# Kernel tuning notes

Measured on AMD Instinct MI355X. Metric: run time of the kernel, lower is better.

## Reference

```python
import jax, jax.numpy as jnp
from jax import lax
import numpy as np

T, B, P, A = 1000, 8192, 1024, 4
ER_DECAY = 1.0 - 1e-3  # per-trial exploration-rate decay


def setup_inputs() -> dict:
    key = jax.random.key(0)
    k1, k2, k3, k4 = jax.random.split(key, 4)
    params = jax.random.normal(k1, (13, P), dtype=jnp.float32) * 0.5
    choices = jax.random.randint(k2, (T, B), 0, A, dtype=jnp.int32)
    rewards = (jax.random.uniform(k3, (T, B)) < 0.5).astype(jnp.float32)
    pids = jax.random.randint(k4, (B,), 0, P, dtype=jnp.int32)
    return {"params": params, "rewards": rewards, "choices": choices, "pids": pids}


def _transform_params(params, pids):
    p = jnp.clip(params, -5.0, 5.0)
    sp, sg = jax.nn.softplus, jax.nn.sigmoid
    beta_r = jnp.clip(sp(p[0]), 0.01, 20.0)[pids]
    lapse = jnp.clip(sg(p[1]), 0.01, 0.99)[pids]
    prior = jnp.clip(sp(p[2]), 0.01, 0.99)[pids]
    alpha_er = jnp.clip(sg(p[3]), 0.01, 0.99)[pids]
    decay = jnp.clip(sg(p[4]), 0.01, 0.99)[pids]
    ab1 = p[5][pids]
    ab2 = p[6][pids]
    perv = sp(p[7])[pids]
    sw = p[8][pids]
    gam = sp(p[10])[pids]
    temp = jnp.clip(sp(p[11]) + 1e-6, 1e-6, 100.0)[pids]
    beta_p = sp(p[12])[pids]
    return beta_r, lapse, prior, alpha_er, decay, ab1, ab2, perv, sw, gam, temp, beta_p


def _forward(params, rewards, choices, pids):
    (beta_r, lapse, prior, alpha_er, decay, ab1, ab2,
     perv, sw, gam, temp, beta_p) = _transform_params(params, pids)
    nB = rewards.shape[1]

    q0 = prior[:, None] * jnp.ones((nB, A), dtype=rewards.dtype)
    carry0 = (q0,
              -jnp.ones((nB,), jnp.int32),          # old_choice
              jnp.zeros((nB,), rewards.dtype),       # trials since last switch
              alpha_er,                              # exploration rate
              jnp.zeros((nB, A), rewards.dtype))     # cumulative choice counts

    def step(carry, xs):
        q, old_choice, tsls, er, cum = carry
        choice, reward = xs                       # (B,), (B,)
        oh = jax.nn.one_hot(choice, A, dtype=q.dtype)        # (B, A)
        target = reward - gam * (1.0 - reward)                # loss-averse target
        q = q * (1.0 - oh) + oh * target[:, None]             # q[choice] = target
        same = choice == old_choice
        tsls = jnp.where(same, tsls + 1.0, 0.0)
        er = er * ER_DECAY
        cum = cum + oh
        # exploration smoothing toward mean, then decay
        q = (1.0 - er)[:, None] * q + er[:, None] * q.mean(-1, keepdims=True)
        q = q * decay[:, None]
        sm_in = beta_r[:, None] * q / temp[:, None] + beta_p[:, None] * jnp.log1p(cum)
        probs = (1.0 - lapse)[:, None] * jax.nn.softmax(sm_in, axis=-1) + lapse[:, None] / A
        cl = jnp.log(probs)
        samef = same.astype(q.dtype)[:, None]
        cl = (cl
              + samef * perv[:, None] * oh
              + (1.0 - samef) * sw[:, None] * oh
              + ab1[:, None] * jax.nn.one_hot(old_choice, A, dtype=q.dtype)  # old_choice=-1 -> zeros
              + ab2[:, None] * jax.nn.one_hot((choice + 2) % A, A, dtype=q.dtype)
              + oh * jnp.log(tsls + 1.0)[:, None])
        return (q, choice, tsls, er, cum), cl

    _, logits = lax.scan(step, carry0, (choices, rewards))
    return logits  # (T, B, A)


def reference(params, rewards, choices, pids):
    return _forward(params, rewards, choices, pids)
```

## Files before the change

kernel.cpp:

```cpp
#include <hip/hip_runtime.h>
#include <stdint.h>

#define T_TRIALS 1000
#define B_SIZE   8192
#define P_SIZE   1024
#define CHUNK    32
#define KCH      32
#define NM       31
#define BPB      16
#define BP       17
#define ER_DECAY 0.999f
#define ER_L2D   (-1.4434228e-3f)
#define LOG2E_F 1.4426950408889634f
#define LN2_F   0.69314718055994531f

typedef float f32x4_t __attribute__((ext_vector_type(4)));

__device__ __forceinline__ float sp_(float x){ return __logf(1.0f + __expf(x)); }
__device__ __forceinline__ float sg_(float x){ return 1.0f / (1.0f + __expf(-x)); }
__device__ __forceinline__ float clampf(float x, float lo, float hi){ return fminf(fmaxf(x, lo), hi); }

__global__ __launch_bounds__(512)
void castro_fused4(const float* __restrict__ params,
                   const float* __restrict__ rewards,
                   const int*   __restrict__ choices,
                   const int*   __restrict__ pids,
                   float4*      __restrict__ out4)
{
    __shared__ float4   smap0[NM][BP];
    __shared__ float4   smap1[NM][BP];
    __shared__ float4   smap2[NM][BP];
    __shared__ float4   smap3[NM][BP];
    __shared__ float4   smap4[NM][BP];
    __shared__ uint32_t smeta[NM][BP];
    __shared__ float    pshare[BPB][10];

    const int tid = threadIdx.x;
    const int k   = tid >> 4;
    const int bi  = tid & 15;
    const int b   = blockIdx.x * BPB + bi;
    const int t0  = k * CHUNK;
    const int pid = pids[b];

    const float p3  = clampf(params[ 3 * P_SIZE + pid], -5.0f, 5.0f);
    const float p4  = clampf(params[ 4 * P_SIZE + pid], -5.0f, 5.0f);
    const float p10 = clampf(params[10 * P_SIZE + pid], -5.0f, 5.0f);
    const float alpha_er = clampf(sg_(p3), 0.01f, 0.99f);
    const float decay    = clampf(sg_(p4), 0.01f, 0.99f);
    const float gam      = sp_(p10);
    const float gp1      = 1.0f + gam;

    if (tid < BPB) {
        const float q0_ = clampf(params[ 0 * P_SIZE + pid], -5.0f, 5.0f);
        const float q1_ = clampf(params[ 1 * P_SIZE + pid], -5.0f, 5.0f);
        const float q2_ = clampf(params[ 2 * P_SIZE + pid], -5.0f, 5.0f);
        const float q5_ = clampf(params[ 5 * P_SIZE + pid], -5.0f, 5.0f);
        const float q6_ = clampf(params[ 6 * P_SIZE + pid], -5.0f, 5.0f);
        const float q7_ = clampf(params[ 7 * P_SIZE + pid], -5.0f, 5.0f);
        const float q8_ = clampf(params[ 8 * P_SIZE + pid], -5.0f, 5.0f);
        const float q11 = clampf(params[11 * P_SIZE + pid], -5.0f, 5.0f);
        const float q12 = clampf(params[12 * P_SIZE + pid], -5.0f, 5.0f);
        const float beta_r = clampf(sp_(q0_), 0.01f, 20.0f);
        const float lapse  = clampf(sg_(q1_), 0.01f, 0.99f);
        const float prior  = clampf(sp_(q2_), 0.01f, 0.99f);
        const float temp   = clampf(sp_(q11) + 1e-6f, 1e-6f, 100.0f);
        pshare[tid][0] = (beta_r / temp) * LOG2E_F;
        pshare[tid][1] = 1.0f - lapse;
        pshare[tid][2] = 0.25f * lapse;
        pshare[tid][3] = prior;
        pshare[tid][4] = sp_(q7_);
        pshare[tid][5] = q8_;
        pshare[tid][6] = q5_;
        pshare[tid][7] = q6_;
        pshare[tid][8] = sp_(q12);
        pshare[tid][9] = 0.0f;
    }

    const int*   cp = choices + (size_t)t0 * B_SIZE + b;
    const float* rp = rewards + (size_t)t0 * B_SIZE + b;

    uint32_t wr[4] = {0u, 0u, 0u, 0u};

    if (k < NM) {
        float er = alpha_er * exp2f((float)t0 * ER_L2D);

        float m00=1.f,m01=0.f,m02=0.f,m03=0.f;
        float m10=0.f,m11=1.f,m12=0.f,m13=0.f;
        float m20=0.f,m21=0.f,m22=1.f,m23=0.f;
        float m30=0.f,m31=0.f,m32=0.f,m33=1.f;
        float b0=0.f,b1=0.f,b2=0.f,b3=0.f;
        int   c1=0,c2=0,c3=0;
        int   run=0, last=-1;

        int cbuf[8]; float rbuf[8];
        #pragma unroll
        for (int i = 0; i < 8; ++i) {
            cbuf[i] = cp[(size_t)i * B_SIZE];
            rbuf[i] = rp[(size_t)i * B_SIZE];
        }

        #pragma unroll
        for (int g = 0; g < 4; ++g) {
            int cc[8]; float rr[8];
            #pragma unroll
            for (int i = 0; i < 8; ++i) { cc[i]=cbuf[i]; rr[i]=rbuf[i]; }
            if (g < 3) {
                #pragma unroll
                for (int i = 0; i < 8; ++i) {
                    cbuf[i] = cp[(size_t)((g+1)*8 + i) * B_SIZE];
                    rbuf[i] = rp[(size_t)((g+1)*8 + i) * B_SIZE];
                }
            }
            uint32_t gw = 0;
            #pragma unroll
            for (int i = 0; i < 8; ++i) {
                const int   c = cc[i];
                const float r = rr[i];
                gw |= ((uint32_t)c | (r > 0.5f ? 4u : 0u)) << (4*i);

                er *= ER_DECAY;
                const float target = fmaf(r, gp1, -gam);
                const bool e0=(c==0), e1=(c==1), e2=(c==2), e3=(c==3);

                m00=e0?0.f:m00; m01=e0?0.f:m01; m02=e0?0.f:m02; m03=e0?0.f:m03; b0=e0?target:b0;
                m10=e1?0.f:m10; m11=e1?0.f:m11; m12=e1?0.f:m12; m13=e1?0.f:m13; b1=e1?target:b1;
                m20=e2?0.f:m20; m21=e2?0.f:m21; m22=e2?0.f:m22; m23=e2?0.f:m23; b2=e2?target:b2;
                m30=e3?0.f:m30; m31=e3?0.f:m31; m32=e3?0.f:m32; m33=e3?0.f:m33; b3=e3?target:b3;

                const float s0=(m00+m10)+(m20+m30);
                const float s1=(m01+m11)+(m21+m31);
                const float s2=(m02+m12)+(m22+m32);
                const float s3=(m03+m13)+(m23+m33);
                const float sb=(b0+b1)+(b2+b3);
                const float a  = decay * (1.0f - er);
                const float e4 = decay * er * 0.25f;

                m00=fmaf(e4,s0,a*m00); m01=fmaf(e4,s1,a*m01); m02=fmaf(e4,s2,a*m02); m03=fmaf(e4,s3,a*m03);
                m10=fmaf(e4,s0,a*m10); m11=fmaf(e4,s1,a*m11); m12=fmaf(e4,s2,a*m12); m13=fmaf(e4,s3,a*m13);
                m20=fmaf(e4,s0,a*m20); m21=fmaf(e4,s1,a*m21); m22=fmaf(e4,s2,a*m22); m23=fmaf(e4,s3,a*m23);
                m30=fmaf(e4,s0,a*m30); m31=fmaf(e4,s1,a*m31); m32=fmaf(e4,s2,a*m32); m33=fmaf(e4,s3,a*m33);
                b0=fmaf(e4,sb,a*b0); b1=fmaf(e4,sb,a*b1); b2=fmaf(e4,sb,a*b2); b3=fmaf(e4,sb,a*b3);

                c1 += e1; c2 += e2; c3 += e3;
                run = (c == last) ? run + 1 : 1;
                last = c;
            }
            wr[g] = gw;
        }

        smap0[k][bi] = make_float4(m00,m01,m02,m03);
        smap1[k][bi] = make_float4(m10,m11,m12,m13);
        smap2[k][bi] = make_float4(m20,m21,m22,m23);
        smap3[k][bi] = make_float4(m30,m31,m32,m33);
        smap4[k][bi] = make_float4(b0,b1,b2,b3);
        smeta[k][bi] = (uint32_t)c1 | ((uint32_t)c2<<6) | ((uint32_t)c3<<12)
                     | ((uint32_t)last<<18) | ((uint32_t)run<<20);
    } else {
        uint32_t gw = 0;
        #pragma unroll
        for (int i = 0; i < 8; ++i) {
            const int   c = cp[(size_t)i * B_SIZE];
            const float r = rp[(size_t)i * B_SIZE];
            gw |= ((uint32_t)c | (r > 0.5f ? 4u : 0u)) << (4*i);
        }
        wr[0] = gw;
    }

    __syncthreads();

    if (tid < BPB) {
        const float prior = pshare[tid][3];
        float q0=prior, q1=prior, q2=prior, q3=prior;
        int n0=0,n1=0,n2=0,n3=0;
        int g_run=0, g_last=-1;

        for (int k2 = 0; k2 < KCH; ++k2) {
            if (k2 > 0) {
                const int tsls = g_run - 1;
                smap0[k2-1][tid] = make_float4(q0,q1,q2,q3);
                smap1[k2-1][tid] = make_float4(0.0f,
                                               __int_as_float(n0 | (n1<<16)),
                                               __int_as_float(n2 | (n3<<16)),
                                               __int_as_float((tsls & 0xFFFF) | (g_last<<16)));
            }
            if (k2 < NM) {
                const float4 r0 = smap0[k2][tid];
                const float4 r1 = smap1[k2][tid];
                const float4 r2 = smap2[k2][tid];
                const float4 r3 = smap3[k2][tid];
                const float4 r4 = smap4[k2][tid];
                const uint32_t m = smeta[k2][tid];
                const float nq0 = fmaf(r0.w,q3, fmaf(r0.z,q2, fmaf(r0.y,q1, fmaf(r0.x,q0, r4.x))));
                const float nq1 = fmaf(r1.w,q3, fmaf(r1.z,q2, fmaf(r1.y,q1, fmaf(r1.x,q0, r4.y))));
                const float nq2 = fmaf(r2.w,q3, fmaf(r2.z,q2, fmaf(r2.y,q1, fmaf(r2.x,q0, r4.z))));
                const float nq3 = fmaf(r3.w,q3, fmaf(r3.z,q2, fmaf(r3.y,q1, fmaf(r3.x,q0, r4.w))));
                q0=nq0; q1=nq1; q2=nq2; q3=nq3;

                const int cc1 = (int)( m        & 63u);
                const int cc2 = (int)((m >> 6 ) & 63u);
                const int cc3 = (int)((m >> 12) & 63u);
                n0 += CHUNK - cc1 - cc2 - cc3;
                n1 += cc1; n2 += cc2; n3 += cc3;
                const int last = (int)((m >> 18) & 3u);
                const int rn   = (int)((m >> 20) & 63u);
                g_run  = (rn == CHUNK && last == g_last) ? g_run + CHUNK : rn;
                g_last = last;
            }
        }
    }
    __syncthreads();

    {
        const float bt2    = pshare[bi][0];
        const float ol     = pshare[bi][1];
        const float la4    = pshare[bi][2];
        const float prior  = pshare[bi][3];
        const float perv   = pshare[bi][4];
        const float sw     = pshare[bi][5];
        const float ab1    = pshare[bi][6];
        const float ab2    = pshare[bi][7];
        const float beta_p = pshare[bi][8];

        float q0,q1,q2,q3, ft;
        float f0,f1,f2,f3;
        int   old_c;
        if (k == 0) {
            q0=q1=q2=q3=prior; f0=f1=f2=f3=0.f; ft=0.f; old_c=-1;
        } else {
            const float4 sA = smap0[k-1][bi];
            const float4 sB = smap1[k-1][bi];
            q0=sA.x; q1=sA.y; q2=sA.z; q3=sA.w;
            const int u1 = __float_as_int(sB.y);
            const int u2 = __float_as_int(sB.z);
            const int u3 = __float_as_int(sB.w);
            f0 = (float)(u1 & 0xFFFF); f1 = (float)(u1 >> 16);
            f2 = (float)(u2 & 0xFFFF); f3 = (float)(u2 >> 16);
            ft = (float)(u3 & 0xFFFF);
            old_c = u3 >> 16;
        }
        float er = alpha_er * exp2f((float)t0 * ER_L2D);

        float bpl0 = beta_p * __log2f(1.0f + f0);
        float bpl1 = beta_p * __log2f(1.0f + f1);
        float bpl2 = beta_p * __log2f(1.0f + f2);
        float bpl3 = beta_p * __log2f(1.0f + f3);

        float4* op = out4 + (size_t)t0 * B_SIZE + b;
        const int ngroups = (k == NM) ? 1 : 4;

        #pragma unroll
        for (int g = 0; g < 4; ++g) {
            if (g < ngroups) {
                uint32_t word = wr[g];
                #pragma unroll
                for (int i = 0; i < 8; ++i) {
                    const int   code = (int)(word & 0xFu); word >>= 4;
                    const int   c    = code & 3;
                    const float r    = (float)((code >> 2) & 1);

                    const float target = fmaf(r, gp1, -gam);
                    const bool e0=(c==0), e1=(c==1), e2=(c==2), e3=(c==3);
                    q0 = e0 ? target : q0;
                    q1 = e1 ? target : q1;
                    q2 = e2 ? target : q2;
                    q3 = e3 ? target : q3;

                    const bool same = (c == old_c);
                    ft = same ? ft + 1.0f : 0.0f;
                    er *= ER_DECAY;

                    const float fsel = e0 ? f0 : (e1 ? f1 : (e2 ? f2 : f3));
                    const float bplc = beta_p * __log2f(fsel + 2.0f);
                    f0 += e0 ? 1.0f : 0.0f;
                    f1 += e1 ? 1.0f : 0.0f;
                    f2 += e2 ? 1.0f : 0.0f;
                    f3 += e3 ? 1.0f : 0.0f;
                    bpl0 = e0 ? bplc : bpl0;
                    bpl1 = e1 ? bplc : bpl1;
                    bpl2 = e2 ? bplc : bpl2;
                    bpl3 = e3 ? bplc : bpl3;

                    const float qm = 0.25f * ((q0+q1)+(q2+q3));
                    q0 = decay * fmaf(er, qm - q0, q0);
                    q1 = decay * fmaf(er, qm - q1, q1);
                    q2 = decay * fmaf(er, qm - q2, q2);
                    q3 = decay * fmaf(er, qm - q3, q3);

                    const float s0 = fmaf(bt2, q0, bpl0);
                    const float s1 = fmaf(bt2, q1, bpl1);
                    const float s2 = fmaf(bt2, q2, bpl2);
                    const float s3 = fmaf(bt2, q3, bpl3);

                    const float m  = fmaxf(fmaxf(s0, s1), fmaxf(s2, s3));
                    const float x0 = exp2f(s0 - m);
                    const float x1 = exp2f(s1 - m);
                    const float x2 = exp2f(s2 - m);
                    const float x3 = exp2f(s3 - m);
                    const float inv = __builtin_amdgcn_rcpf((x0+x1)+(x2+x3));
                    const float sc  = ol * inv;

                    const float L0 = __log2f(fmaf(sc, x0, la4));
                    const float L1 = __log2f(fmaf(sc, x1, la4));
                    const float L2 = __log2f(fmaf(sc, x2, la4));
                    const float L3 = __log2f(fmaf(sc, x3, la4));

                    const float bonus = fmaf(LN2_F, __log2f(ft + 1.0f), same ? perv : sw);

                    float a0 = (e0 ? bonus : 0.0f) + ((old_c == 0) ? ab1 : 0.0f);
                    float a1 = (e1 ? bonus : 0.0f) + ((old_c == 1) ? ab1 : 0.0f);
                    float a2 = (e2 ? bonus : 0.0f) + ((old_c == 2) ? ab1 : 0.0f);
                    float a3 = (e3 ? bonus : 0.0f) + ((old_c == 3) ? ab1 : 0.0f);
                    const int c2 = (c + 2) & 3;
                    a0 += (c2 == 0) ? ab2 : 0.0f;
                    a1 += (c2 == 1) ? ab2 : 0.0f;
                    a2 += (c2 == 2) ? ab2 : 0.0f;
                    a3 += (c2 == 3) ? ab2 : 0.0f;

                    f32x4_t v = { fmaf(LN2_F, L0, a0), fmaf(LN2_F, L1, a1),
                                  fmaf(LN2_F, L2, a2), fmaf(LN2_F, L3, a3) };
                    __builtin_nontemporal_store(v,
                        reinterpret_cast<f32x4_t*>(op + (size_t)(g*8 + i) * B_SIZE));
                    old_c = c;
                }
            }
        }
    }
}

extern "C" void kernel_launch(void* const* d_in, const int* in_sizes, int n_in,
                              void* d_out, int out_size, void* d_ws, size_t ws_size,
                              hipStream_t stream)
{
    const float* params  = (const float*)d_in[0];
    const float* rewards = (const float*)d_in[1];
    const int*   choices = (const int*)  d_in[2];
    const int*   pids    = (const int*)  d_in[3];

    hipLaunchKernelGGL(castro_fused4, dim3(B_SIZE/BPB), dim3(512), 0, stream,
                       params, rewards, choices, pids, (float4*)d_out);
}
```

Before: 62.25 us.

## Add 1024-thread kernel with 16-trial chunks and dynamic LDS scan

Adds a new kernel that splits the 1000-trial scan into 16-trial chunks across 1024 threads per block (63 chunk-threads per batch element). Each chunk builds an affine transition map that a single thread composes serially, followed by a parallel replay that writes the logits. The host raises the dynamic shared memory limit to about 80 KB and falls back to the old 512-thread kernel if that call fails. Halving the chunk length shortens the per-thread serial replay, but it doubles the length of the serial composition and raises LDS use, which may lower occupancy.

```diff
diff --git a/kernel.cpp b/kernel.cpp
--- a/kernel.cpp
+++ b/kernel.cpp
@@ -4,21 +4,390 @@
 #define T_TRIALS 1000
 #define B_SIZE   8192
 #define P_SIZE   1024
+#define ER_DECAY 0.999f
+#define ER_L2D   (-1.4434228e-3f)
+#define LOG2E_F 1.4426950408889634f
+#define LN2_F   0.69314718055994531f
+
+typedef float f32x4_t __attribute__((ext_vector_type(4)));
+
+__device__ __forceinline__ float sp_(float x){ return __logf(1.0f + __expf(x)); }
+__device__ __forceinline__ float sg_(float x){ return 1.0f / (1.0f + __expf(-x)); }
+__device__ __forceinline__ float clampf(float x, float lo, float hi){ return fminf(fmaxf(x, lo), hi); }
+
+#define F5_CHUNK  16
+#define F5_NMST   60
+#define F5_LDS_BYTES 81536
+
+__global__ __launch_bounds__(1024, 8)
+void castro_fused5(const float* __restrict__ params,
+                   const float* __restrict__ rewards,
+                   const int*   __restrict__ choices,
+                   const int*   __restrict__ pids,
+                   float4*      __restrict__ out4)
+{
+    extern __shared__ char lds_raw[];
+    float4*   smap0  = (float4*)lds_raw;
+    float4*   smap1  = smap0 + 960;
+    float4*   smap2  = smap1 + 960;
+    float4*   smap3  = smap2 + 960;
+    float4*   smap4  = smap3 + 960;
+    uint32_t* smeta  = (uint32_t*)(smap4 + 960);
+    float*    pshare = (float*)(smeta + 960);
+    uint32_t* tailw  = (uint32_t*)(pshare + 160);
+
+    const int tid = threadIdx.x;
+    const int k   = tid >> 4;
+    const int bi  = tid & 15;
+    const int b   = blockIdx.x * 16 + bi;
+    const int t0  = k * F5_CHUNK;
+    const int pid = pids[b];
+
+    const float p3  = clampf(params[ 3 * P_SIZE + pid], -5.0f, 5.0f);
+    const float p4  = clampf(params[ 4 * P_SIZE + pid], -5.0f, 5.0f);
+    const float p10 = clampf(params[10 * P_SIZE + pid], -5.0f, 5.0f);
+    const float alpha_er = clampf(sg_(p3), 0.01f, 0.99f);
+    const float decay    = clampf(sg_(p4), 0.01f, 0.99f);
+    const float gam      = sp_(p10);
+    const float gp1      = 1.0f + gam;
+
+    if (tid < 16) {
+        const float q0_ = clampf(params[ 0 * P_SIZE + pid], -5.0f, 5.0f);
+        const float q1_ = clampf(params[ 1 * P_SIZE + pid], -5.0f, 5.0f);
+        const float q2_ = clampf(params[ 2 * P_SIZE + pid], -5.0f, 5.0f);
+        const float q5_ = clampf(params[ 5 * P_SIZE + pid], -5.0f, 5.0f);
+        const float q6_ = clampf(params[ 6 * P_SIZE + pid], -5.0f, 5.0f);
+        const float q7_ = clampf(params[ 7 * P_SIZE + pid], -5.0f, 5.0f);
+        const float q8_ = clampf(params[ 8 * P_SIZE + pid], -5.0f, 5.0f);
+        const float q11 = clampf(params[11 * P_SIZE + pid], -5.0f, 5.0f);
+        const float q12 = clampf(params[12 * P_SIZE + pid], -5.0f, 5.0f);
+        const float beta_r = clampf(sp_(q0_), 0.01f, 20.0f);
+        const float lapse  = clampf(sg_(q1_), 0.01f, 0.99f);
+        const float prior  = clampf(sp_(q2_), 0.01f, 0.99f);
+        const float temp   = clampf(sp_(q11) + 1e-6f, 1e-6f, 100.0f);
+        float* ps = pshare + tid * 10;
+        ps[0] = (beta_r / temp) * LOG2E_F;
+        ps[1] = 1.0f - lapse;
+        ps[2] = 0.25f * lapse;
+        ps[3] = prior;
+        ps[4] = sp_(q7_);
+        ps[5] = q8_;
+        ps[6] = q5_;
+        ps[7] = q6_;
+        ps[8] = sp_(q12);
+        ps[9] = 0.0f;
+    }
+
+    const int*   cp = choices + (size_t)t0 * B_SIZE + b;
+    const float* rp = rewards + (size_t)t0 * B_SIZE + b;
+
+    uint32_t wr[2] = {0u, 0u};
+
+    if (k < F5_NMST) {
+        float er = alpha_er * exp2f((float)t0 * ER_L2D);
+
+        float m00=1.f,m01=0.f,m02=0.f,m03=0.f;
+        float m10=0.f,m11=1.f,m12=0.f,m13=0.f;
+        float m20=0.f,m21=0.f,m22=1.f,m23=0.f;
+        float m30=0.f,m31=0.f,m32=0.f,m33=1.f;
+        float b0=0.f,b1=0.f,b2=0.f,b3=0.f;
+        int   c1=0,c2=0,c3=0;
+        int   run=0, last=-1;
+
+        int cbuf[8]; float rbuf[8];
+        #pragma unroll
+        for (int i = 0; i < 8; ++i) {
+            cbuf[i] = cp[(size_t)i * B_SIZE];
+            rbuf[i] = rp[(size_t)i * B_SIZE];
+        }
+
+        #pragma unroll
+        for (int g = 0; g < 2; ++g) {
+            int cc[8]; float rr[8];
+            #pragma unroll
+            for (int i = 0; i < 8; ++i) { cc[i]=cbuf[i]; rr[i]=rbuf[i]; }
+            if (g < 1) {
+                #pragma unroll
+                for (int i = 0; i < 8; ++i) {
+                    cbuf[i] = cp[(size_t)(8 + i) * B_SIZE];
+                    rbuf[i] = rp[(size_t)(8 + i) * B_SIZE];
+                }
+            }
+            uint32_t gw = 0;
+            #pragma unroll
+            for (int i = 0; i < 8; ++i) {
+                const int   c = cc[i];
+                const float r = rr[i];
+                gw |= ((uint32_t)c | (r > 0.5f ? 4u : 0u)) << (4*i);
+
+                er *= ER_DECAY;
+                const float target = fmaf(r, gp1, -gam);
+                const bool e0=(c==0), e1=(c==1), e2=(c==2), e3=(c==3);
+
+                m00=e0?0.f:m00; m01=e0?0.f:m01; m02=e0?0.f:m02; m03=e0?0.f:m03; b0=e0?target:b0;
+                m10=e1?0.f:m10; m11=e1?0.f:m11; m12=e1?0.f:m12; m13=e1?0.f:m13; b1=e1?target:b1;
+                m20=e2?0.f:m20; m21=e2?0.f:m21; m22=e2?0.f:m22; m23=e2?0.f:m23; b2=e2?target:b2;
+                m30=e3?0.f:m30; m31=e3?0.f:m31; m32=e3?0.f:m32; m33=e3?0.f:m33; b3=e3?target:b3;
+
+                const float s0=(m00+m10)+(m20+m30);
+                const float s1=(m01+m11)+(m21+m31);
+                const float s2=(m02+m12)+(m22+m32);
+                const float s3=(m03+m13)+(m23+m33);
+                const float sb=(b0+b1)+(b2+b3);
+                const float a  = decay * (1.0f - er);
+                const float e4 = decay * er * 0.25f;
+
+                m00=fmaf(e4,s0,a*m00); m01=fmaf(e4,s1,a*m01); m02=fmaf(e4,s2,a*m02); m03=fmaf(e4,s3,a*m03);
+                m10=fmaf(e4,s0,a*m10); m11=fmaf(e4,s1,a*m11); m12=fmaf(e4,s2,a*m12); m13=fmaf(e4,s3,a*m13);
+                m20=fmaf(e4,s0,a*m20); m21=fmaf(e4,s1,a*m21); m22=fmaf(e4,s2,a*m22); m23=fmaf(e4,s3,a*m23);
+                m30=fmaf(e4,s0,a*m30); m31=fmaf(e4,s1,a*m31); m32=fmaf(e4,s2,a*m32); m33=fmaf(e4,s3,a*m33);
+                b0=fmaf(e4,sb,a*b0); b1=fmaf(e4,sb,a*b1); b2=fmaf(e4,sb,a*b2); b3=fmaf(e4,sb,a*b3);
+
+                c1 += e1; c2 += e2; c3 += e3;
+                run = (c == last) ? run + 1 : 1;
+                last = c;
+            }
+            wr[g] = gw;
+        }
+
+        const int si = k * 16 + bi;
+        smap0[si] = make_float4(m00,m01,m02,m03);
+        smap1[si] = make_float4(m10,m11,m12,m13);
+        smap2[si] = make_float4(m20,m21,m22,m23);
+        smap3[si] = make_float4(m30,m31,m32,m33);
+        smap4[si] = make_float4(b0,b1,b2,b3);
+        smeta[si] = (uint32_t)c1 | ((uint32_t)c2<<6) | ((uint32_t)c3<<12)
+                  | ((uint32_t)last<<18) | ((uint32_t)run<<20);
+    } else if (k < 62) {
+        #pragma unroll
+        for (int g = 0; g < 2; ++g) {
+            uint32_t gw = 0;
+            #pragma unroll
+            for (int i = 0; i < 8; ++i) {
+                const int   c = cp[(size_t)(g*8 + i) * B_SIZE];
+                const float r = rp[(size_t)(g*8 + i) * B_SIZE];
+                gw |= ((uint32_t)c | (r > 0.5f ? 4u : 0u)) << (4*i);
+            }
+            wr[g] = gw;
+            tailw[((k - 60)*2 + g) * 16 + bi] = gw;
+        }
+    } else if (k == 62) {
+        uint32_t gw = 0;
+        #pragma unroll
+        for (int i = 0; i < 8; ++i) {
+            const int   c = cp[(size_t)i * B_SIZE];
+            const float r = rp[(size_t)i * B_SIZE];
+            gw |= ((uint32_t)c | (r > 0.5f ? 4u : 0u)) << (4*i);
+        }
+        wr[0] = gw;
+    }
+
+    __syncthreads();
+
+    if (tid < 16) {
+        const float prior = pshare[tid*10 + 3];
+        float q0=prior, q1=prior, q2=prior, q3=prior;
+        int n0=0,n1=0,n2=0,n3=0;
+        int g_run=0, g_last=-1;
+
+        for (int k2 = 0; k2 <= F5_NMST; ++k2) {
+            if (k2 > 0) {
+                const int tsls = g_run - 1;
+                const int si = (k2-1)*16 + tid;
+                smap0[si] = make_float4(q0,q1,q2,q3);
+                smap1[si] = make_float4(0.0f,
+                                        __int_as_float(n0 | (n1<<16)),
+                                        __int_as_float(n2 | (n3<<16)),
+                                        __int_as_float((tsls & 0xFFFF) | (g_last<<16)));
+            }
+            if (k2 < F5_NMST) {
+                const int si = k2*16 + tid;
+                const float4 r0 = smap0[si];
+                const float4 r1 = smap1[si];
+                const float4 r2 = smap2[si];
+                const float4 r3 = smap3[si];
+                const float4 r4 = smap4[si];
+                const uint32_t m = smeta[si];
+                const float nq0 = fmaf(r0.w,q3, fmaf(r0.z,q2, fmaf(r0.y,q1, fmaf(r0.x,q0, r4.x))));
+                const float nq1 = fmaf(r1.w,q3, fmaf(r1.z,q2, fmaf(r1.y,q1, fmaf(r1.x,q0, r4.y))));
+                const float nq2 = fmaf(r2.w,q3, fmaf(r2.z,q2, fmaf(r2.y,q1, fmaf(r2.x,q0, r4.z))));
+                const float nq3 = fmaf(r3.w,q3, fmaf(r3.z,q2, fmaf(r3.y,q1, fmaf(r3.x,q0, r4.w))));
+                q0=nq0; q1=nq1; q2=nq2; q3=nq3;
+
+                const int cc1 = (int)( m        & 63u);
+                const int cc2 = (int)((m >> 6 ) & 63u);
+                const int cc3 = (int)((m >> 12) & 63u);
+                n0 += F5_CHUNK - cc1 - cc2 - cc3;
+                n1 += cc1; n2 += cc2; n3 += cc3;
+                const int last = (int)((m >> 18) & 3u);
+                const int rn   = (int)((m >> 20) & 63u);
+                g_run  = (rn == F5_CHUNK && last == g_last) ? g_run + F5_CHUNK : rn;
+                g_last = last;
+            }
+        }
+    }
+    __syncthreads();
+
+    if (k < 63) {
+        const float* ps = pshare + bi * 10;
+        const float bt2    = ps[0];
+        const float ol     = ps[1];
+        const float la4    = ps[2];
+        const float prior  = ps[3];
+        const float perv   = ps[4];
+        const float sw     = ps[5];
+        const float ab1    = ps[6];
+        const float ab2    = ps[7];
+        const float beta_p = ps[8];
+
+        float q0,q1,q2,q3, ft;
+        float f0,f1,f2,f3;
+        int   old_c;
+        float er;
+
+        if (k == 0) {
+            q0=q1=q2=q3=prior; f0=f1=f2=f3=0.f; ft=0.f; old_c=-1;
+            er = alpha_er;
+        } else {
+            const int row = (k <= F5_NMST) ? (k-1) : (F5_NMST-1);
+            const float4 sA = smap0[row*16 + bi];
+            const float4 sB = smap1[row*16 + bi];
+            q0=sA.x; q1=sA.y; q2=sA.z; q3=sA.w;
+            const int u1 = __float_as_int(sB.y);
+            const int u2 = __float_as_int(sB.z);
+            const int u3 = __float_as_int(sB.w);
+            f0 = (float)(u1 & 0xFFFF); f1 = (float)(u1 >> 16);
+            f2 = (float)(u2 & 0xFFFF); f3 = (float)(u2 >> 16);
+            ft = (float)(u3 & 0xFFFF);
+            old_c = u3 >> 16;
+            const int t_state = (k <= F5_NMST) ? t0 : (F5_NMST * F5_CHUNK);
+            er = alpha_er * exp2f((float)t_state * ER_L2D);
+        }
+
+        if (k > F5_NMST) {
+            const int nrep = (k - F5_NMST) * 2;
+            for (int w = 0; w < nrep; ++w) {
+                uint32_t word = tailw[w*16 + bi];
+                #pragma unroll
+                for (int i = 0; i < 8; ++i) {
+                    const int   code = (int)(word & 0xFu); word >>= 4;
+                    const int   c    = code & 3;
+                    const float r    = (float)((code >> 2) & 1);
+                    const float target = fmaf(r, gp1, -gam);
+                    const bool e0=(c==0), e1=(c==1), e2=(c==2), e3=(c==3);
+                    q0 = e0 ? target : q0;
+                    q1 = e1 ? target : q1;
+                    q2 = e2 ? target : q2;
+                    q3 = e3 ? target : q3;
+                    const bool same = (c == old_c);
+                    ft = same ? ft + 1.0f : 0.0f;
+                    er *= ER_DECAY;
+                    f0 += e0 ? 1.0f : 0.0f;
+                    f1 += e1 ? 1.0f : 0.0f;
+                    f2 += e2 ? 1.0f : 0.0f;
+                    f3 += e3 ? 1.0f : 0.0f;
+                    const float qm = 0.25f * ((q0+q1)+(q2+q3));
+                    q0 = decay * fmaf(er, qm - q0, q0);
+                    q1 = decay * fmaf(er, qm - q1, q1);
+                    q2 = decay * fmaf(er, qm - q2, q2);
+                    q3 = decay * fmaf(er, qm - q3, q3);
+                    old_c = c;
+                }
+            }
+        }
+
+        float bpl0 = beta_p * __log2f(1.0f + f0);
+        float bpl1 = beta_p * __log2f(1.0f + f1);
+        float bpl2 = beta_p * __log2f(1.0f + f2);
+        float bpl3 = beta_p * __log2f(1.0f + f3);
+
+        float4* op = out4 + (size_t)t0 * B_SIZE + b;
+        const int ngroups = (k == 62) ? 1 : 2;
+
+        #pragma unroll
+        for (int g = 0; g < 2; ++g) {
+            if (g < ngroups) {
+                uint32_t word = wr[g];
+                #pragma unroll
+                for (int i = 0; i < 8; ++i) {
+                    const int   code = (int)(word & 0xFu); word >>= 4;
+                    const int   c    = code & 3;
+                    const float r    = (float)((code >> 2) & 1);
+
+                    const float target = fmaf(r, gp1, -gam);
+                    const bool e0=(c==0), e1=(c==1), e2=(c==2), e3=(c==3);
+                    q0 = e0 ? target : q0;
+                    q1 = e1 ? target : q1;
+                    q2 = e2 ? target : q2;
+                    q3 = e3 ? target : q3;
+
+                    const bool same = (c == old_c);
+                    ft = same ? ft + 1.0f : 0.0f;
+                    er *= ER_DECAY;
+
+                    const float fsel = e0 ? f0 : (e1 ? f1 : (e2 ? f2 : f3));
+                    const float bplc = beta_p * __log2f(fsel + 2.0f);
+                    f0 += e0 ? 1.0f : 0.0f;
+                    f1 += e1 ? 1.0f : 0.0f;
+                    f2 += e2 ? 1.0f : 0.0f;
+                    f3 += e3 ? 1.0f : 0.0f;
+                    bpl0 = e0 ? bplc : bpl0;
+                    bpl1 = e1 ? bplc : bpl1;
+                    bpl2 = e2 ? bplc : bpl2;
+                    bpl3 = e3 ? bplc : bpl3;
+
+                    const float qm = 0.25f * ((q0+q1)+(q2+q3));
+                    q0 = decay * fmaf(er, qm - q0, q0);
+                    q1 = decay * fmaf(er, qm - q1, q1);
+                    q2 = decay * fmaf(er, qm - q2, q2);
+                    q3 = decay * fmaf(er, qm - q3, q3);
+
+                    const float s0 = fmaf(bt2, q0, bpl0);
+                    const float s1 = fmaf(bt2, q1, bpl1);
+                    const float s2 = fmaf(bt2, q2, bpl2);
+                    const float s3 = fmaf(bt2, q3, bpl3);
+
+                    const float m  = fmaxf(fmaxf(s0, s1), fmaxf(s2, s3));
+                    const float x0 = exp2f(s0 - m);
+                    const float x1 = exp2f(s1 - m);
+                    const float x2 = exp2f(s2 - m);
+                    const float x3 = exp2f(s3 - m);
+                    const float inv = __builtin_amdgcn_rcpf((x0+x1)+(x2+x3));
+                    const float sc  = ol * inv;
+
+                    const float L0 = __log2f(fmaf(sc, x0, la4));
+                    const float L1 = __log2f(fmaf(sc, x1, la4));
+                    const float L2 = __log2f(fmaf(sc, x2, la4));
+                    const float L3 = __log2f(fmaf(sc, x3, la4));
+
+                    const float bonus = fmaf(LN2_F, __log2f(ft + 1.0f), same ? perv : sw);
+
+                    float a0 = (e0 ? bonus : 0.0f) + ((old_c == 0) ? ab1 : 0.0f);
+                    float a1 = (e1 ? bonus : 0.0f) + ((old_c == 1) ? ab1 : 0.0f);
+                    float a2 = (e2 ? bonus : 0.0f) + ((old_c == 2) ? ab1 : 0.0f);
+                    float a3 = (e3 ? bonus : 0.0f) + ((old_c == 3) ? ab1 : 0.0f);
+                    const int c2 = (c + 2) & 3;
+                    a0 += (c2 == 0) ? ab2 : 0.0f;
+                    a1 += (c2 == 1) ? ab2 : 0.0f;
+                    a2 += (c2 == 2) ? ab2 : 0.0f;
+                    a3 += (c2 == 3) ? ab2 : 0.0f;
+
+                    f32x4_t v = { fmaf(LN2_F, L0, a0), fmaf(LN2_F, L1, a1),
+                                  fmaf(LN2_F, L2, a2), fmaf(LN2_F, L3, a3) };
+                    __builtin_nontemporal_store(v,
+                        reinterpret_cast<f32x4_t*>(op + (size_t)(g*8 + i) * B_SIZE));
+                    old_c = c;
+                }
+            }
+        }
+    }
+}
+
 #define CHUNK    32
 #define KCH      32
 #define NM       31
 #define BPB      16
 #define BP       17
-#define ER_DECAY 0.999f
-#define ER_L2D   (-1.4434228e-3f)
-#define LOG2E_F 1.4426950408889634f
-#define LN2_F   0.69314718055994531f
-
-typedef float f32x4_t __attribute__((ext_vector_type(4)));
-
-__device__ __forceinline__ float sp_(float x){ return __logf(1.0f + __expf(x)); }
-__device__ __forceinline__ float sg_(float x){ return 1.0f / (1.0f + __expf(-x)); }
-__device__ __forceinline__ float clampf(float x, float lo, float hi){ return fminf(fmaxf(x, lo), hi); }
 
 __global__ __launch_bounds__(512)
 void castro_fused4(const float* __restrict__ params,
@@ -336,6 +705,16 @@
     const int*   choices = (const int*)  d_in[2];
     const int*   pids    = (const int*)  d_in[3];
 
-    hipLaunchKernelGGL(castro_fused4, dim3(B_SIZE/BPB), dim3(512), 0, stream,
-                       params, rewards, choices, pids, (float4*)d_out);
+    hipError_t e = hipFuncSetAttribute(
+        reinterpret_cast<const void*>(castro_fused5),
+        hipFuncAttributeMaxDynamicSharedMemorySize, F5_LDS_BYTES);
+
+    if (e == hipSuccess) {
+        hipLaunchKernelGGL(castro_fused5, dim3(B_SIZE/16), dim3(1024),
+                           F5_LDS_BYTES, stream,
+                           params, rewards, choices, pids, (float4*)d_out);
+    } else {
+        hipLaunchKernelGGL(castro_fused4, dim3(B_SIZE/16), dim3(512), 0, stream,
+                           params, rewards, choices, pids, (float4*)d_out);
+    }
 }
```

New measurement: 80.83 us. +29.9%, slower.

## Use packed FP32 math and a shared log2 lookup table in scan kernel

Applied to the files above, without the earlier changes.

Rewrites the 4x4 affine-map composition and the per-step softmax/log path to use two-wide float vectors with elementwise FMA, so the compiler can emit packed FP32 instructions (v_pk_fma_f32) on CDNA. Choice counts and the switch run length become integers, and their log2 values are read from a 1024-entry shared-memory table instead of computed with transcendental instructions. The reward target becomes a select instead of an FMA. In exchange, every block fills the table on entry, adds LDS lookups, and may add register pressure or repacking moves if the compiler does not pair lanes cleanly.

```diff
diff --git a/kernel.cpp b/kernel.cpp
--- a/kernel.cpp
+++ b/kernel.cpp
@@ -15,13 +15,15 @@
 #define LN2_F   0.69314718055994531f
 
 typedef float f32x4_t __attribute__((ext_vector_type(4)));
+typedef float f32x2_t __attribute__((ext_vector_type(2)));
 
 __device__ __forceinline__ float sp_(float x){ return __logf(1.0f + __expf(x)); }
 __device__ __forceinline__ float sg_(float x){ return 1.0f / (1.0f + __expf(-x)); }
 __device__ __forceinline__ float clampf(float x, float lo, float hi){ return fminf(fmaxf(x, lo), hi); }
+__device__ __forceinline__ f32x2_t pkfma(f32x2_t a, f32x2_t b, f32x2_t c){ return __builtin_elementwise_fma(a, b, c); }
 
 __global__ __launch_bounds__(512)
-void castro_fused4(const float* __restrict__ params,
+void castro_fused6(const float* __restrict__ params,
                    const float* __restrict__ rewards,
                    const int*   __restrict__ choices,
                    const int*   __restrict__ pids,
@@ -34,6 +36,7 @@
     __shared__ float4   smap4[NM][BP];
     __shared__ uint32_t smeta[NM][BP];
     __shared__ float    pshare[BPB][10];
+    __shared__ float    ltab[1024];
 
     const int tid = threadIdx.x;
     const int k   = tid >> 4;
@@ -42,13 +45,17 @@
     const int t0  = k * CHUNK;
     const int pid = pids[b];
 
+    #pragma unroll
+    for (int i = tid; i < 1024; i += 512)
+        ltab[i] = __log2f((float)(i < 1 ? 1 : i));
+
     const float p3  = clampf(params[ 3 * P_SIZE + pid], -5.0f, 5.0f);
     const float p4  = clampf(params[ 4 * P_SIZE + pid], -5.0f, 5.0f);
     const float p10 = clampf(params[10 * P_SIZE + pid], -5.0f, 5.0f);
     const float alpha_er = clampf(sg_(p3), 0.01f, 0.99f);
     const float decay    = clampf(sg_(p4), 0.01f, 0.99f);
     const float gam      = sp_(p10);
-    const float gp1      = 1.0f + gam;
+    const float ngam     = -gam;
 
     if (tid < BPB) {
         const float q0_ = clampf(params[ 0 * P_SIZE + pid], -5.0f, 5.0f);
@@ -84,11 +91,12 @@
     if (k < NM) {
         float er = alpha_er * exp2f((float)t0 * ER_L2D);
 
-        float m00=1.f,m01=0.f,m02=0.f,m03=0.f;
-        float m10=0.f,m11=1.f,m12=0.f,m13=0.f;
-        float m20=0.f,m21=0.f,m22=1.f,m23=0.f;
-        float m30=0.f,m31=0.f,m32=0.f,m33=1.f;
-        float b0=0.f,b1=0.f,b2=0.f,b3=0.f;
+        f32x2_t r0l = {1.f,0.f}, r0h = {0.f,0.f};
+        f32x2_t r1l = {0.f,1.f}, r1h = {0.f,0.f};
+        f32x2_t r2l = {0.f,0.f}, r2h = {1.f,0.f};
+        f32x2_t r3l = {0.f,0.f}, r3h = {0.f,1.f};
+        f32x2_t b01 = {0.f,0.f}, b23 = {0.f,0.f};
+        const f32x2_t zz = {0.f,0.f};
         int   c1=0,c2=0,c3=0;
         int   run=0, last=-1;
 
@@ -114,32 +122,34 @@
             uint32_t gw = 0;
             #pragma unroll
             for (int i = 0; i < 8; ++i) {
-                const int   c = cc[i];
-                const float r = rr[i];
-                gw |= ((uint32_t)c | (r > 0.5f ? 4u : 0u)) << (4*i);
+                const int  c    = cc[i];
+                const bool rbit = (rr[i] > 0.5f);
+                gw |= ((uint32_t)c | (rbit ? 4u : 0u)) << (4*i);
 
                 er *= ER_DECAY;
-                const float target = fmaf(r, gp1, -gam);
+                const float target = rbit ? 1.0f : ngam;
                 const bool e0=(c==0), e1=(c==1), e2=(c==2), e3=(c==3);
 
-                m00=e0?0.f:m00; m01=e0?0.f:m01; m02=e0?0.f:m02; m03=e0?0.f:m03; b0=e0?target:b0;
-                m10=e1?0.f:m10; m11=e1?0.f:m11; m12=e1?0.f:m12; m13=e1?0.f:m13; b1=e1?target:b1;
-                m20=e2?0.f:m20; m21=e2?0.f:m21; m22=e2?0.f:m22; m23=e2?0.f:m23; b2=e2?target:b2;
-                m30=e3?0.f:m30; m31=e3?0.f:m31; m32=e3?0.f:m32; m33=e3?0.f:m33; b3=e3?target:b3;
-
-                const float s0=(m00+m10)+(m20+m30);
-                const float s1=(m01+m11)+(m21+m31);
-                const float s2=(m02+m12)+(m22+m32);
-                const float s3=(m03+m13)+(m23+m33);
-                const float sb=(b0+b1)+(b2+b3);
+                r0l = e0 ? zz : r0l;  r0h = e0 ? zz : r0h;  b01.x = e0 ? target : b01.x;
+                r1l = e1 ? zz : r1l;  r1h = e1 ? zz : r1h;  b01.y = e1 ? target : b01.y;
+                r2l = e2 ? zz : r2l;  r2h = e2 ? zz : r2h;  b23.x = e2 ? target : b23.x;
+                r3l = e3 ? zz : r3l;  r3h = e3 ? zz : r3h;  b23.y = e3 ? target : b23.y;
+
+                const f32x2_t sl = (r0l + r1l) + (r2l + r3l);
+                const f32x2_t sh = (r0h + r1h) + (r2h + r3h);
+                const f32x2_t sbv = b01 + b23;
+                const float   sb  = sbv.x + sbv.y;
                 const float a  = decay * (1.0f - er);
                 const float e4 = decay * er * 0.25f;
-
-                m00=fmaf(e4,s0,a*m00); m01=fmaf(e4,s1,a*m01); m02=fmaf(e4,s2,a*m02); m03=fmaf(e4,s3,a*m03);
-                m10=fmaf(e4,s0,a*m10); m11=fmaf(e4,s1,a*m11); m12=fmaf(e4,s2,a*m12); m13=fmaf(e4,s3,a*m13);
-                m20=fmaf(e4,s0,a*m20); m21=fmaf(e4,s1,a*m21); m22=fmaf(e4,s2,a*m22); m23=fmaf(e4,s3,a*m23);
-                m30=fmaf(e4,s0,a*m30); m31=fmaf(e4,s1,a*m31); m32=fmaf(e4,s2,a*m32); m33=fmaf(e4,s3,a*m33);
-                b0=fmaf(e4,sb,a*b0); b1=fmaf(e4,sb,a*b1); b2=fmaf(e4,sb,a*b2); b3=fmaf(e4,sb,a*b3);
+                const f32x2_t av  = {a, a};
+                const f32x2_t e4v = {e4, e4};
+                const f32x2_t sbp = {sb, sb};
+
+                r0l = pkfma(e4v, sl, r0l*av);  r0h = pkfma(e4v, sh, r0h*av);
+                r1l = pkfma(e4v, sl, r1l*av);  r1h = pkfma(e4v, sh, r1h*av);
+                r2l = pkfma(e4v, sl, r2l*av);  r2h = pkfma(e4v, sh, r2h*av);
+                r3l = pkfma(e4v, sl, r3l*av);  r3h = pkfma(e4v, sh, r3h*av);
+                b01 = pkfma(e4v, sbp, b01*av); b23 = pkfma(e4v, sbp, b23*av);
 
                 c1 += e1; c2 += e2; c3 += e3;
                 run = (c == last) ? run + 1 : 1;
@@ -148,11 +158,11 @@
             wr[g] = gw;
         }
 
-        smap0[k][bi] = make_float4(m00,m01,m02,m03);
-        smap1[k][bi] = make_float4(m10,m11,m12,m13);
-        smap2[k][bi] = make_float4(m20,m21,m22,m23);
-        smap3[k][bi] = make_float4(m30,m31,m32,m33);
-        smap4[k][bi] = make_float4(b0,b1,b2,b3);
+        smap0[k][bi] = make_float4(r0l.x, r0l.y, r0h.x, r0h.y);
+        smap1[k][bi] = make_float4(r1l.x, r1l.y, r1h.x, r1h.y);
+        smap2[k][bi] = make_float4(r2l.x, r2l.y, r2h.x, r2h.y);
+        smap3[k][bi] = make_float4(r3l.x, r3l.y, r3h.x, r3h.y);
+        smap4[k][bi] = make_float4(b01.x, b01.y, b23.x, b23.y);
         smeta[k][bi] = (uint32_t)c1 | ((uint32_t)c2<<6) | ((uint32_t)c3<<12)
                      | ((uint32_t)last<<18) | ((uint32_t)run<<20);
     } else {
@@ -221,29 +231,31 @@
         const float ab2    = pshare[bi][7];
         const float beta_p = pshare[bi][8];
 
-        float q0,q1,q2,q3, ft;
-        float f0,f1,f2,f3;
-        int   old_c;
+        f32x2_t q01, q23;
+        int   n0,n1,n2,n3, ft_i, old_c;
         if (k == 0) {
-            q0=q1=q2=q3=prior; f0=f1=f2=f3=0.f; ft=0.f; old_c=-1;
+            q01 = (f32x2_t){prior, prior}; q23 = q01;
+            n0=n1=n2=n3=0; ft_i=0; old_c=-1;
         } else {
             const float4 sA = smap0[k-1][bi];
             const float4 sB = smap1[k-1][bi];
-            q0=sA.x; q1=sA.y; q2=sA.z; q3=sA.w;
+            q01 = (f32x2_t){sA.x, sA.y}; q23 = (f32x2_t){sA.z, sA.w};
             const int u1 = __float_as_int(sB.y);
             const int u2 = __float_as_int(sB.z);
             const int u3 = __float_as_int(sB.w);
-            f0 = (float)(u1 & 0xFFFF); f1 = (float)(u1 >> 16);
-            f2 = (float)(u2 & 0xFFFF); f3 = (float)(u2 >> 16);
-            ft = (float)(u3 & 0xFFFF);
+            n0 = u1 & 0xFFFF; n1 = u1 >> 16;
+            n2 = u2 & 0xFFFF; n3 = u2 >> 16;
+            ft_i = u3 & 0xFFFF;
             old_c = u3 >> 16;
         }
         float er = alpha_er * exp2f((float)t0 * ER_L2D);
 
-        float bpl0 = beta_p * __log2f(1.0f + f0);
-        float bpl1 = beta_p * __log2f(1.0f + f1);
-        float bpl2 = beta_p * __log2f(1.0f + f2);
-        float bpl3 = beta_p * __log2f(1.0f + f3);
+        f32x2_t bpl01 = { beta_p * ltab[n0 + 1], beta_p * ltab[n1 + 1] };
+        f32x2_t bpl23 = { beta_p * ltab[n2 + 1], beta_p * ltab[n3 + 1] };
+
+        const f32x2_t bt2v = {bt2, bt2};
+        const f32x2_t la4v = {la4, la4};
+        const f32x2_t ln2v = {LN2_F, LN2_F};
 
         float4* op = out4 + (size_t)t0 * B_SIZE + b;
         const int ngroups = (k == NM) ? 1 : 4;
@@ -254,57 +266,59 @@
                 uint32_t word = wr[g];
                 #pragma unroll
                 for (int i = 0; i < 8; ++i) {
-                    const int   code = (int)(word & 0xFu); word >>= 4;
-                    const int   c    = code & 3;
-                    const float r    = (float)((code >> 2) & 1);
-
-                    const float target = fmaf(r, gp1, -gam);
+                    const int code = (int)(word & 0xFu); word >>= 4;
+                    const int c    = code & 3;
+                    const float target = (code & 4) ? 1.0f : ngam;
                     const bool e0=(c==0), e1=(c==1), e2=(c==2), e3=(c==3);
-                    q0 = e0 ? target : q0;
-                    q1 = e1 ? target : q1;
-                    q2 = e2 ? target : q2;
-                    q3 = e3 ? target : q3;
+
+                    q01.x = e0 ? target : q01.x;
+                    q01.y = e1 ? target : q01.y;
+                    q23.x = e2 ? target : q23.x;
+                    q23.y = e3 ? target : q23.y;
 
                     const bool same = (c == old_c);
-                    ft = same ? ft + 1.0f : 0.0f;
+                    ft_i = same ? ft_i + 1 : 0;
                     er *= ER_DECAY;
 
-                    const float fsel = e0 ? f0 : (e1 ? f1 : (e2 ? f2 : f3));
-                    const float bplc = beta_p * __log2f(fsel + 2.0f);
-                    f0 += e0 ? 1.0f : 0.0f;
-                    f1 += e1 ? 1.0f : 0.0f;
-                    f2 += e2 ? 1.0f : 0.0f;
-                    f3 += e3 ? 1.0f : 0.0f;
-                    bpl0 = e0 ? bplc : bpl0;
-                    bpl1 = e1 ? bplc : bpl1;
-                    bpl2 = e2 ? bplc : bpl2;
-                    bpl3 = e3 ? bplc : bpl3;
-
-                    const float qm = 0.25f * ((q0+q1)+(q2+q3));
-                    q0 = decay * fmaf(er, qm - q0, q0);
-                    q1 = decay * fmaf(er, qm - q1, q1);
-                    q2 = decay * fmaf(er, qm - q2, q2);
-                    q3 = decay * fmaf(er, qm - q3, q3);
-
-                    const float s0 = fmaf(bt2, q0, bpl0);
-                    const float s1 = fmaf(bt2, q1, bpl1);
-                    const float s2 = fmaf(bt2, q2, bpl2);
-                    const float s3 = fmaf(bt2, q3, bpl3);
-
-                    const float m  = fmaxf(fmaxf(s0, s1), fmaxf(s2, s3));
-                    const float x0 = exp2f(s0 - m);
-                    const float x1 = exp2f(s1 - m);
-                    const float x2 = exp2f(s2 - m);
-                    const float x3 = exp2f(s3 - m);
+                    const int nsel = e0 ? n0 : (e1 ? n1 : (e2 ? n2 : n3));
+                    const float bplc = beta_p * ltab[nsel + 2];
+                    n0 += e0; n1 += e1; n2 += e2; n3 += e3;
+                    bpl01.x = e0 ? bplc : bpl01.x;
+                    bpl01.y = e1 ? bplc : bpl01.y;
+                    bpl23.x = e2 ? bplc : bpl23.x;
+                    bpl23.y = e3 ? bplc : bpl23.y;
+
+                    const f32x2_t qs = q01 + q23;
+                    const float   qm = 0.25f * (qs.x + qs.y);
+                    const f32x2_t qmv = {qm, qm};
+                    const f32x2_t erv = {er, er};
+                    const f32x2_t dcv = {decay, decay};
+                    q01 = pkfma(erv, qmv - q01, q01) * dcv;
+                    q23 = pkfma(erv, qmv - q23, q23) * dcv;
+
+                    const f32x2_t s01 = pkfma(bt2v, q01, bpl01);
+                    const f32x2_t s23 = pkfma(bt2v, q23, bpl23);
+
+                    const float m = fmaxf(fmaxf(s01.x, s01.y), fmaxf(s23.x, s23.y));
+                    const f32x2_t mv = {m, m};
+                    const f32x2_t d01 = s01 - mv;
+                    const f32x2_t d23 = s23 - mv;
+                    const float x0 = exp2f(d01.x);
+                    const float x1 = exp2f(d01.y);
+                    const float x2 = exp2f(d23.x);
+                    const float x3 = exp2f(d23.y);
                     const float inv = __builtin_amdgcn_rcpf((x0+x1)+(x2+x3));
                     const float sc  = ol * inv;
-
-                    const float L0 = __log2f(fmaf(sc, x0, la4));
-                    const float L1 = __log2f(fmaf(sc, x1, la4));
-                    const float L2 = __log2f(fmaf(sc, x2, la4));
-                    const float L3 = __log2f(fmaf(sc, x3, la4));
-
-                    const float bonus = fmaf(LN2_F, __log2f(ft + 1.0f), same ? perv : sw);
+                    const f32x2_t scv = {sc, sc};
+
+                    const f32x2_t y01 = pkfma(scv, (f32x2_t){x0,x1}, la4v);
+                    const f32x2_t y23 = pkfma(scv, (f32x2_t){x2,x3}, la4v);
+                    const float L0 = __log2f(y01.x);
+                    const float L1 = __log2f(y01.y);
+                    const float L2 = __log2f(y23.x);
+                    const float L3 = __log2f(y23.y);
+
+                    const float bonus = fmaf(LN2_F, ltab[ft_i + 1], same ? perv : sw);
 
                     float a0 = (e0 ? bonus : 0.0f) + ((old_c == 0) ? ab1 : 0.0f);
                     float a1 = (e1 ? bonus : 0.0f) + ((old_c == 1) ? ab1 : 0.0f);
@@ -316,8 +330,10 @@
                     a2 += (c2 == 2) ? ab2 : 0.0f;
                     a3 += (c2 == 3) ? ab2 : 0.0f;
 
-                    f32x4_t v = { fmaf(LN2_F, L0, a0), fmaf(LN2_F, L1, a1),
-                                  fmaf(LN2_F, L2, a2), fmaf(LN2_F, L3, a3) };
+                    const f32x2_t o01 = pkfma(ln2v, (f32x2_t){L0,L1}, (f32x2_t){a0,a1});
+                    const f32x2_t o23 = pkfma(ln2v, (f32x2_t){L2,L3}, (f32x2_t){a2,a3});
+
+                    f32x4_t v = { o01.x, o01.y, o23.x, o23.y };
                     __builtin_nontemporal_store(v,
                         reinterpret_cast<f32x4_t*>(op + (size_t)(g*8 + i) * B_SIZE));
                     old_c = c;
@@ -336,6 +352,6 @@
     const int*   choices = (const int*)  d_in[2];
     const int*   pids    = (const int*)  d_in[3];
 
-    hipLaunchKernelGGL(castro_fused4, dim3(B_SIZE/BPB), dim3(512), 0, stream,
+    hipLaunchKernelGGL(castro_fused6, dim3(B_SIZE/BPB), dim3(512), 0, stream,
                        params, rewards, choices, pids, (float4*)d_out);
 }
```

Measured after the change: 66.48 us. 1.07x slower.
